# Performance work log

Hardware: AMD Instinct MI355X
Metric: run time of the kernel (lower is better)

Reference implementation:

```python
import jax, jax.numpy as jnp
import numpy as np

N, E, D, C = 40000, 640000, 128, 64


def setup_inputs() -> dict:
    key = jax.random.key(0)
    ks = jax.random.split(key, 12)
    x = jax.random.normal(ks[0], (N, D), dtype=jnp.float32)
    edge_row = jax.random.randint(ks[1], (E,), 0, N, dtype=jnp.int32)
    edge_col = jax.random.randint(ks[2], (E,), 0, N, dtype=jnp.int32)
    edge_val = jax.random.uniform(ks[3], (E,), dtype=jnp.float32)
    s1 = 1.0 / np.sqrt(D)
    W1 = jax.random.uniform(ks[4], (D, D), minval=-s1, maxval=s1, dtype=jnp.float32)
    b1 = jax.random.uniform(ks[5], (D,), minval=-s1, maxval=s1, dtype=jnp.float32)
    W2 = jax.random.uniform(ks[6], (D, D), minval=-s1, maxval=s1, dtype=jnp.float32)
    b2 = jax.random.uniform(ks[7], (D,), minval=-s1, maxval=s1, dtype=jnp.float32)
    Wf = jax.random.uniform(ks[8], (D, C), minval=-s1, maxval=s1, dtype=jnp.float32)
    bf = jax.random.uniform(ks[9], (C,), minval=-s1, maxval=s1, dtype=jnp.float32)
    return {"x": x, "edge_row": edge_row, "edge_col": edge_col, "edge_val": edge_val,
            "W1": W1, "b1": b1, "W2": W2, "b2": b2, "Wf": Wf, "bf": bf}


def _spmm(row, col, val, dense):
    # out[row] += val * dense[col]  == adj @ dense with adj in COO form
    msgs = dense[col] * val[:, None]  # [E, D]
    return jax.ops.segment_sum(msgs, row, num_segments=N)


def reference(x, edge_row, edge_col, edge_val, W1, b1, W2, b2, Wf, bf):
    # gc1: relu(adj @ (x @ W1) + b1)
    h = jax.nn.relu(_spmm(edge_row, edge_col, edge_val, x @ W1) + b1)
    # dropout(p=0.2, training=False) -> identity in eval mode
    # gc2 + residual: relu(adj @ (h @ W2) + b2) + h
    h2 = jax.nn.relu(_spmm(edge_row, edge_col, edge_val, h @ W2) + b2) + h
    # final linear classifier
    return h2 @ Wf + bf
```

## Files before the change

### kernel.cpp

```cpp
#include <hip/hip_runtime.h>

#define N_NODES 40000
#define N_EDGES 640000
#define DIM     128
#define NCLS    64
#define CAP     64
#define CSTRIDE 16

typedef __attribute__((ext_vector_type(8))) short short8v;
typedef __attribute__((ext_vector_type(4))) float f32x4;

__device__ __forceinline__ unsigned short f2bf(float f) {
    unsigned int u = __float_as_uint(f);
    unsigned int r = u + 0x7fffu + ((u >> 16) & 1u);
    return (unsigned short)(r >> 16);
}
__device__ __forceinline__ float bf2f(unsigned int s) {
    return __uint_as_float(s << 16);
}
__device__ __forceinline__ float4 dec4(uint2 u) {
    return make_float4(bf2f(u.x & 0xffffu), bf2f(u.x >> 16),
                       bf2f(u.y & 0xffffu), bf2f(u.y >> 16));
}

__launch_bounds__(256)
__global__ void prep(const float* __restrict__ W1, const float* __restrict__ W2,
                     const float* __restrict__ Wf,
                     unsigned short* __restrict__ wt1, unsigned short* __restrict__ wt2,
                     unsigned short* __restrict__ wtf, int* __restrict__ counts) {
    const int b = blockIdx.x, tid = threadIdx.x;
    if (b < 2500) {
        counts[b * 256 + tid] = 0;
    } else if (b < 2564) {
        int e = (b - 2500) * 256 + tid;
        int k = e >> 7, n = e & 127;
        wt1[n * 128 + k] = f2bf(W1[e]);
    } else if (b < 2628) {
        int e = (b - 2564) * 256 + tid;
        int k = e >> 7, n = e & 127;
        wt2[n * 128 + k] = f2bf(W2[e]);
    } else {
        int e = (b - 2628) * 256 + tid;
        int k = e >> 6, n = e & 63;
        wtf[n * 128 + k] = f2bf(Wf[e]);
    }
}

__launch_bounds__(256)
__global__ void build_bucket(const int4* __restrict__ erow4, const int4* __restrict__ ecol4,
                             const float4* __restrict__ ev4, int* __restrict__ counts,
                             uint2* __restrict__ bslot) {
    int t = blockIdx.x * 256 + threadIdx.x;
    int4   r = erow4[t];
    int4   c = ecol4[t];
    float4 v = ev4[t];
    int p0 = atomicAdd(&counts[r.x * CSTRIDE], 1);
    int p1 = atomicAdd(&counts[r.y * CSTRIDE], 1);
    int p2 = atomicAdd(&counts[r.z * CSTRIDE], 1);
    int p3 = atomicAdd(&counts[r.w * CSTRIDE], 1);
    if (p0 < CAP) bslot[(size_t)r.x * CAP + p0] = make_uint2((unsigned)c.x, __float_as_uint(v.x));
    if (p1 < CAP) bslot[(size_t)r.y * CAP + p1] = make_uint2((unsigned)c.y, __float_as_uint(v.y));
    if (p2 < CAP) bslot[(size_t)r.z * CAP + p2] = make_uint2((unsigned)c.z, __float_as_uint(v.z));
    if (p3 < CAP) bslot[(size_t)r.w * CAP + p3] = make_uint2((unsigned)c.w, __float_as_uint(v.w));
}

__launch_bounds__(256)
__global__ void gemm_f32A_bf16(const float* __restrict__ A,
                               const unsigned short* __restrict__ WT,
                               unsigned short* __restrict__ C) {
    __shared__ unsigned short sB[128 * 128];
    const int tid = threadIdx.x;
    for (int c = tid; c < 2048; c += 256) {
        int n = c >> 4, j = c & 15;
        short8v v = *reinterpret_cast<const short8v*>(WT + n * 128 + 8 * j);
        *reinterpret_cast<short8v*>(&sB[n * 128 + 8 * (j ^ (n & 7))]) = v;
    }
    __syncthreads();

    const int lane = tid & 63;
    const int wv   = tid >> 6;
    const int m0   = blockIdx.x * 64 + wv * 16;
    const int r    = lane & 15;
    const int g    = lane >> 4;

    short8v af[4];
    const float* arow = A + (size_t)(m0 + r) * 128 + 8 * g;
#pragma unroll
    for (int f = 0; f < 4; ++f) {
        float4 p = *reinterpret_cast<const float4*>(arow + 32 * f);
        float4 q = *reinterpret_cast<const float4*>(arow + 32 * f + 4);
        short8v a;
        a[0] = (short)f2bf(p.x); a[1] = (short)f2bf(p.y);
        a[2] = (short)f2bf(p.z); a[3] = (short)f2bf(p.w);
        a[4] = (short)f2bf(q.x); a[5] = (short)f2bf(q.y);
        a[6] = (short)f2bf(q.z); a[7] = (short)f2bf(q.w);
        af[f] = a;
    }

    f32x4 acc[8];
#pragma unroll
    for (int nt = 0; nt < 8; ++nt) acc[nt] = (f32x4){0.f, 0.f, 0.f, 0.f};

#pragma unroll
    for (int nt = 0; nt < 8; ++nt) {
        const int rw = nt * 16 + r;
        const unsigned short* bbase = &sB[rw * 128];
#pragma unroll
        for (int f = 0; f < 4; ++f) {
            short8v bfr = *reinterpret_cast<const short8v*>(bbase + 8 * ((4 * f + g) ^ (rw & 7)));
            acc[nt] = __builtin_amdgcn_mfma_f32_16x16x32_bf16(af[f], bfr, acc[nt], 0, 0, 0);
        }
    }
#pragma unroll
    for (int nt = 0; nt < 8; ++nt)
#pragma unroll
        for (int rr = 0; rr < 4; ++rr)
            C[(size_t)(m0 + g * 4 + rr) * 128 + nt * 16 + r] = f2bf(acc[nt][rr]);
}

__launch_bounds__(256)
__global__ void gemm_bf16_128(const unsigned short* __restrict__ A,
                              const unsigned short* __restrict__ WT,
                              unsigned short* __restrict__ C) {
    __shared__ unsigned short sB[128 * 128];
    const int tid = threadIdx.x;
    for (int c = tid; c < 2048; c += 256) {
        int n = c >> 4, j = c & 15;
        short8v v = *reinterpret_cast<const short8v*>(WT + n * 128 + 8 * j);
        *reinterpret_cast<short8v*>(&sB[n * 128 + 8 * (j ^ (n & 7))]) = v;
    }
    __syncthreads();

    const int lane = tid & 63;
    const int wv   = tid >> 6;
    const int m0   = blockIdx.x * 64 + wv * 16;
    const int r    = lane & 15;
    const int g    = lane >> 4;

    short8v af[4];
    const unsigned short* arow = A + (size_t)(m0 + r) * 128 + 8 * g;
#pragma unroll
    for (int f = 0; f < 4; ++f)
        af[f] = *reinterpret_cast<const short8v*>(arow + 32 * f);

    f32x4 acc[8];
#pragma unroll
    for (int nt = 0; nt < 8; ++nt) acc[nt] = (f32x4){0.f, 0.f, 0.f, 0.f};

#pragma unroll
    for (int nt = 0; nt < 8; ++nt) {
        const int rw = nt * 16 + r;
        const unsigned short* bbase = &sB[rw * 128];
#pragma unroll
        for (int f = 0; f < 4; ++f) {
            short8v bfr = *reinterpret_cast<const short8v*>(bbase + 8 * ((4 * f + g) ^ (rw & 7)));
            acc[nt] = __builtin_amdgcn_mfma_f32_16x16x32_bf16(af[f], bfr, acc[nt], 0, 0, 0);
        }
    }
#pragma unroll
    for (int nt = 0; nt < 8; ++nt)
#pragma unroll
        for (int rr = 0; rr < 4; ++rr)
            C[(size_t)(m0 + g * 4 + rr) * 128 + nt * 16 + r] = f2bf(acc[nt][rr]);
}

__launch_bounds__(256)
__global__ void gemm_bf16_final(const unsigned short* __restrict__ A,
                                const unsigned short* __restrict__ WT,
                                const float* __restrict__ bias,
                                float* __restrict__ C) {
    __shared__ unsigned short sB[64 * 128];
    const int tid = threadIdx.x;
    for (int c = tid; c < 1024; c += 256) {
        int n = c >> 4, j = c & 15;
        short8v v = *reinterpret_cast<const short8v*>(WT + n * 128 + 8 * j);
        *reinterpret_cast<short8v*>(&sB[n * 128 + 8 * (j ^ (n & 7))]) = v;
    }
    __syncthreads();

    const int lane = tid & 63;
    const int wv   = tid >> 6;
    const int m0   = blockIdx.x * 64 + wv * 16;
    const int r    = lane & 15;
    const int g    = lane >> 4;

    short8v af[4];
    const unsigned short* arow = A + (size_t)(m0 + r) * 128 + 8 * g;
#pragma unroll
    for (int f = 0; f < 4; ++f)
        af[f] = *reinterpret_cast<const short8v*>(arow + 32 * f);

    f32x4 acc[4];
#pragma unroll
    for (int nt = 0; nt < 4; ++nt) acc[nt] = (f32x4){0.f, 0.f, 0.f, 0.f};

#pragma unroll
    for (int nt = 0; nt < 4; ++nt) {
        const int rw = nt * 16 + r;
        const unsigned short* bbase = &sB[rw * 128];
#pragma unroll
        for (int f = 0; f < 4; ++f) {
            short8v bfr = *reinterpret_cast<const short8v*>(bbase + 8 * ((4 * f + g) ^ (rw & 7)));
            acc[nt] = __builtin_amdgcn_mfma_f32_16x16x32_bf16(af[f], bfr, acc[nt], 0, 0, 0);
        }
    }
#pragma unroll
    for (int nt = 0; nt < 4; ++nt)
#pragma unroll
        for (int rr = 0; rr < 4; ++rr)
            C[(size_t)(m0 + g * 4 + rr) * 64 + nt * 16 + r] = acc[nt][rr] + bias[nt * 16 + r];
}

__launch_bounds__(256)
__global__ void spmm_fused_bf16(const uint2* __restrict__ dense2,
                                const uint2* __restrict__ bslot,
                                const int* __restrict__ counts,
                                const float4* __restrict__ bias4,
                                const uint2* __restrict__ residbf,
                                uint2* __restrict__ outbf) {
    const int lane = threadIdx.x & 63;
    const int half = lane >> 5;
    const int sub  = lane & 31;
    const int row  = blockIdx.x * 4 + (threadIdx.x >> 6);
    int deg = counts[row * CSTRIDE];
    if (deg > CAP) deg = CAP;

    int   colr = 0;
    float valr = 0.f;
    if (lane < deg) {
        uint2 s = bslot[(size_t)row * CAP + lane];
        colr = (int)s.x;
        valr = __uint_as_float(s.y);
    }
    const int degUp = (deg + 7) & ~7;

    float ax0 = 0.f, ay0 = 0.f, az0 = 0.f, aw0 = 0.f;
    float ax1 = 0.f, ay1 = 0.f, az1 = 0.f, aw1 = 0.f;
    float ax2 = 0.f, ay2 = 0.f, az2 = 0.f, aw2 = 0.f;
    float ax3 = 0.f, ay3 = 0.f, az3 = 0.f, aw3 = 0.f;
    for (int i = 0; i < degUp; i += 8) {
        int   c0 = __shfl(colr, i + 0 + half); float v0 = __shfl(valr, i + 0 + half);
        int   c1 = __shfl(colr, i + 2 + half); float v1 = __shfl(valr, i + 2 + half);
        int   c2 = __shfl(colr, i + 4 + half); float v2 = __shfl(valr, i + 4 + half);
        int   c3 = __shfl(colr, i + 6 + half); float v3 = __shfl(valr, i + 6 + half);
        uint2 u0 = dense2[(size_t)c0 * 32 + sub];
        uint2 u1 = dense2[(size_t)c1 * 32 + sub];
        uint2 u2 = dense2[(size_t)c2 * 32 + sub];
        uint2 u3 = dense2[(size_t)c3 * 32 + sub];
        float4 d0 = dec4(u0); ax0 += v0 * d0.x; ay0 += v0 * d0.y; az0 += v0 * d0.z; aw0 += v0 * d0.w;
        float4 d1 = dec4(u1); ax1 += v1 * d1.x; ay1 += v1 * d1.y; az1 += v1 * d1.z; aw1 += v1 * d1.w;
        float4 d2 = dec4(u2); ax2 += v2 * d2.x; ay2 += v2 * d2.y; az2 += v2 * d2.z; aw2 += v2 * d2.w;
        float4 d3 = dec4(u3); ax3 += v3 * d3.x; ay3 += v3 * d3.y; az3 += v3 * d3.z; aw3 += v3 * d3.w;
    }
    float sx = (ax0 + ax1) + (ax2 + ax3);
    float sy = (ay0 + ay1) + (ay2 + ay3);
    float sz = (az0 + az1) + (az2 + az3);
    float sw = (aw0 + aw1) + (aw2 + aw3);
    sx += __shfl_xor(sx, 32);
    sy += __shfl_xor(sy, 32);
    sz += __shfl_xor(sz, 32);
    sw += __shfl_xor(sw, 32);

    if (half == 0) {
        float4 bb = bias4[sub];
        sx = fmaxf(sx + bb.x, 0.f);
        sy = fmaxf(sy + bb.y, 0.f);
        sz = fmaxf(sz + bb.z, 0.f);
        sw = fmaxf(sw + bb.w, 0.f);
        if (residbf) {
            float4 rr = dec4(residbf[(size_t)row * 32 + sub]);
            sx += rr.x; sy += rr.y; sz += rr.z; sw += rr.w;
        }
        outbf[(size_t)row * 32 + sub] =
            make_uint2((unsigned)f2bf(sx) | ((unsigned)f2bf(sy) << 16),
                       (unsigned)f2bf(sz) | ((unsigned)f2bf(sw) << 16));
    }
}

extern "C" void kernel_launch(void* const* d_in, const int* in_sizes, int n_in,
                              void* d_out, int out_size, void* d_ws, size_t ws_size,
                              hipStream_t stream) {
    const float* x    = (const float*)d_in[0];
    const int*   erow = (const int*)  d_in[1];
    const int*   ecol = (const int*)  d_in[2];
    const float* ev   = (const float*)d_in[3];
    const float* W1   = (const float*)d_in[4];
    const float* b1   = (const float*)d_in[5];
    const float* W2   = (const float*)d_in[6];
    const float* b2   = (const float*)d_in[7];
    const float* Wf   = (const float*)d_in[8];
    const float* bf   = (const float*)d_in[9];
    float* out = (float*)d_out;

    const size_t MB = 1u << 20;
    char* ws = (char*)d_ws;
    int*            counts = (int*)           (ws + 0 * MB);
    uint2*          bslot  = (uint2*)         (ws + 4 * MB);
    unsigned short* gb     = (unsigned short*)(ws + 25 * MB);
    unsigned short* hb     = (unsigned short*)(ws + 36 * MB);
    unsigned short* h2b    = (unsigned short*)(ws + 47 * MB);
    unsigned short* wt1    = (unsigned short*)(ws + 58 * MB);
    unsigned short* wt2    = (unsigned short*)(ws + 58 * MB + 65536);
    unsigned short* wtf    = (unsigned short*)(ws + 58 * MB + 131072);

    prep<<<2660, 256, 0, stream>>>(W1, W2, Wf, wt1, wt2, wtf, counts);
    build_bucket<<<N_EDGES / 4 / 256, 256, 0, stream>>>(
        (const int4*)erow, (const int4*)ecol, (const float4*)ev, counts, bslot);

    gemm_f32A_bf16<<<N_NODES / 64, 256, 0, stream>>>(x, wt1, gb);
    spmm_fused_bf16<<<N_NODES / 4, 256, 0, stream>>>((const uint2*)gb, bslot, counts,
                                                     (const float4*)b1, nullptr,
                                                     (uint2*)hb);
    gemm_bf16_128<<<N_NODES / 64, 256, 0, stream>>>(hb, wt2, gb);
    spmm_fused_bf16<<<N_NODES / 4, 256, 0, stream>>>((const uint2*)gb, bslot, counts,
                                                     (const float4*)b2, (const uint2*)hb,
                                                     (uint2*)h2b);
    gemm_bf16_final<<<N_NODES / 64, 256, 0, stream>>>(h2b, wtf, bf, out);
}
```

Baseline: 189.7 us.

## Bucket each row's edges into four column-range groups for gather locality

```diff
diff --git a/kernel.cpp b/kernel.cpp
--- a/kernel.cpp
+++ b/kernel.cpp
@@ -4,7 +4,8 @@
 #define N_EDGES 640000
 #define DIM     128
 #define NCLS    64
-#define CAP     64
+#define GCAP    32
+#define NSLOT   128
 #define CSTRIDE 16
 
 typedef __attribute__((ext_vector_type(8))) short short8v;
@@ -54,14 +55,18 @@
     int4   r = erow4[t];
     int4   c = ecol4[t];
     float4 v = ev4[t];
-    int p0 = atomicAdd(&counts[r.x * CSTRIDE], 1);
-    int p1 = atomicAdd(&counts[r.y * CSTRIDE], 1);
-    int p2 = atomicAdd(&counts[r.z * CSTRIDE], 1);
-    int p3 = atomicAdd(&counts[r.w * CSTRIDE], 1);
-    if (p0 < CAP) bslot[(size_t)r.x * CAP + p0] = make_uint2((unsigned)c.x, __float_as_uint(v.x));
-    if (p1 < CAP) bslot[(size_t)r.y * CAP + p1] = make_uint2((unsigned)c.y, __float_as_uint(v.y));
-    if (p2 < CAP) bslot[(size_t)r.z * CAP + p2] = make_uint2((unsigned)c.z, __float_as_uint(v.z));
-    if (p3 < CAP) bslot[(size_t)r.w * CAP + p3] = make_uint2((unsigned)c.w, __float_as_uint(v.w));
+    int g0 = (c.x >= 10000) + (c.x >= 20000) + (c.x >= 30000);
+    int g1 = (c.y >= 10000) + (c.y >= 20000) + (c.y >= 30000);
+    int g2 = (c.z >= 10000) + (c.z >= 20000) + (c.z >= 30000);
+    int g3 = (c.w >= 10000) + (c.w >= 20000) + (c.w >= 30000);
+    int p0 = atomicAdd(&counts[r.x * CSTRIDE + g0], 1);
+    int p1 = atomicAdd(&counts[r.y * CSTRIDE + g1], 1);
+    int p2 = atomicAdd(&counts[r.z * CSTRIDE + g2], 1);
+    int p3 = atomicAdd(&counts[r.w * CSTRIDE + g3], 1);
+    if (p0 < GCAP) bslot[(size_t)r.x * NSLOT + g0 * GCAP + p0] = make_uint2((unsigned)c.x, __float_as_uint(v.x));
+    if (p1 < GCAP) bslot[(size_t)r.y * NSLOT + g1 * GCAP + p1] = make_uint2((unsigned)c.y, __float_as_uint(v.y));
+    if (p2 < GCAP) bslot[(size_t)r.z * NSLOT + g2 * GCAP + p2] = make_uint2((unsigned)c.z, __float_as_uint(v.z));
+    if (p3 < GCAP) bslot[(size_t)r.w * NSLOT + g3 * GCAP + p3] = make_uint2((unsigned)c.w, __float_as_uint(v.w));
 }
 
 __launch_bounds__(256)
@@ -222,13 +227,20 @@
     const int half = lane >> 5;
     const int sub  = lane & 31;
     const int row  = blockIdx.x * 4 + (threadIdx.x >> 6);
-    int deg = counts[row * CSTRIDE];
-    if (deg > CAP) deg = CAP;
+
+    int4 cnt = *reinterpret_cast<const int4*>(&counts[row * CSTRIDE]);
+    const int c0 = min(cnt.x, GCAP), c1 = min(cnt.y, GCAP);
+    const int c2 = min(cnt.z, GCAP), c3 = min(cnt.w, GCAP);
+    const int off1 = c0, off2 = c0 + c1, off3 = c0 + c1 + c2;
+    int deg = off3 + c3;
+    if (deg > 64) deg = 64;
 
     int   colr = 0;
     float valr = 0.f;
     if (lane < deg) {
-        uint2 s = bslot[(size_t)row * CAP + lane];
+        int g = (lane >= off1) + (lane >= off2) + (lane >= off3);
+        int base = (g == 0) ? 0 : ((g == 1) ? off1 : ((g == 2) ? off2 : off3));
+        uint2 s = bslot[(size_t)row * NSLOT + g * GCAP + (lane - base)];
         colr = (int)s.x;
         valr = __uint_as_float(s.y);
     }
@@ -239,14 +251,14 @@
     float ax2 = 0.f, ay2 = 0.f, az2 = 0.f, aw2 = 0.f;
     float ax3 = 0.f, ay3 = 0.f, az3 = 0.f, aw3 = 0.f;
     for (int i = 0; i < degUp; i += 8) {
-        int   c0 = __shfl(colr, i + 0 + half); float v0 = __shfl(valr, i + 0 + half);
-        int   c1 = __shfl(colr, i + 2 + half); float v1 = __shfl(valr, i + 2 + half);
-        int   c2 = __shfl(colr, i + 4 + half); float v2 = __shfl(valr, i + 4 + half);
-        int   c3 = __shfl(colr, i + 6 + half); float v3 = __shfl(valr, i + 6 + half);
-        uint2 u0 = dense2[(size_t)c0 * 32 + sub];
-        uint2 u1 = dense2[(size_t)c1 * 32 + sub];
-        uint2 u2 = dense2[(size_t)c2 * 32 + sub];
-        uint2 u3 = dense2[(size_t)c3 * 32 + sub];
+        int   c0e = __shfl(colr, i + 0 + half); float v0 = __shfl(valr, i + 0 + half);
+        int   c1e = __shfl(colr, i + 2 + half); float v1 = __shfl(valr, i + 2 + half);
+        int   c2e = __shfl(colr, i + 4 + half); float v2 = __shfl(valr, i + 4 + half);
+        int   c3e = __shfl(colr, i + 6 + half); float v3 = __shfl(valr, i + 6 + half);
+        uint2 u0 = dense2[(size_t)c0e * 32 + sub];
+        uint2 u1 = dense2[(size_t)c1e * 32 + sub];
+        uint2 u2 = dense2[(size_t)c2e * 32 + sub];
+        uint2 u3 = dense2[(size_t)c3e * 32 + sub];
         float4 d0 = dec4(u0); ax0 += v0 * d0.x; ay0 += v0 * d0.y; az0 += v0 * d0.z; aw0 += v0 * d0.w;
         float4 d1 = dec4(u1); ax1 += v1 * d1.x; ay1 += v1 * d1.y; az1 += v1 * d1.z; aw1 += v1 * d1.w;
         float4 d2 = dec4(u2); ax2 += v2 * d2.x; ay2 += v2 * d2.y; az2 += v2 * d2.z; aw2 += v2 * d2.w;
@@ -296,12 +308,12 @@
     char* ws = (char*)d_ws;
     int*            counts = (int*)           (ws + 0 * MB);
     uint2*          bslot  = (uint2*)         (ws + 4 * MB);
-    unsigned short* gb     = (unsigned short*)(ws + 25 * MB);
-    unsigned short* hb     = (unsigned short*)(ws + 36 * MB);
-    unsigned short* h2b    = (unsigned short*)(ws + 47 * MB);
-    unsigned short* wt1    = (unsigned short*)(ws + 58 * MB);
-    unsigned short* wt2    = (unsigned short*)(ws + 58 * MB + 65536);
-    unsigned short* wtf    = (unsigned short*)(ws + 58 * MB + 131072);
+    unsigned short* gb     = (unsigned short*)(ws + 46 * MB);
+    unsigned short* hb     = (unsigned short*)(ws + 57 * MB);
+    unsigned short* h2b    = (unsigned short*)(ws + 68 * MB);
+    unsigned short* wt1    = (unsigned short*)(ws + 79 * MB);
+    unsigned short* wt2    = (unsigned short*)(ws + 79 * MB + 65536);
+    unsigned short* wtf    = (unsigned short*)(ws + 79 * MB + 131072);
 
     prep<<<2660, 256, 0, stream>>>(W1, W2, Wf, wt1, wt2, wtf, counts);
     build_bucket<<<N_EDGES / 4 / 256, 256, 0, stream>>>(
```

Measured after the change: 191.8 us. Within noise of the previous version (+1.1%).

## Merge edge bucketing, first GEMM and weight prep into one heterogeneous launch

Applied to the files above, without the earlier changes.

```diff
diff --git a/kernel.cpp b/kernel.cpp
--- a/kernel.cpp
+++ b/kernel.cpp
@@ -7,6 +7,11 @@
 #define CAP     64
 #define CSTRIDE 16
 
+#define NB_BUILD 625
+#define NB_GEMM  625
+#define NB_WT2   64
+#define NB_WTF   32
+
 typedef __attribute__((ext_vector_type(8))) short short8v;
 typedef __attribute__((ext_vector_type(4))) float f32x4;
 
@@ -24,98 +29,93 @@
 }
 
 __launch_bounds__(256)
-__global__ void prep(const float* __restrict__ W1, const float* __restrict__ W2,
-                     const float* __restrict__ Wf,
-                     unsigned short* __restrict__ wt1, unsigned short* __restrict__ wt2,
-                     unsigned short* __restrict__ wtf, int* __restrict__ counts) {
-    const int b = blockIdx.x, tid = threadIdx.x;
-    if (b < 2500) {
-        counts[b * 256 + tid] = 0;
-    } else if (b < 2564) {
-        int e = (b - 2500) * 256 + tid;
-        int k = e >> 7, n = e & 127;
-        wt1[n * 128 + k] = f2bf(W1[e]);
-    } else if (b < 2628) {
-        int e = (b - 2564) * 256 + tid;
+__global__ void prep_wt1(const float* __restrict__ W1, unsigned short* __restrict__ wt1) {
+    int e = blockIdx.x * 256 + threadIdx.x;
+    int k = e >> 7, n = e & 127;
+    wt1[n * 128 + k] = f2bf(W1[e]);
+}
+
+__launch_bounds__(256)
+__global__ void build_and_gemm1(const int4* __restrict__ erow4, const int4* __restrict__ ecol4,
+                                const float4* __restrict__ ev4, int* __restrict__ counts,
+                                uint2* __restrict__ bslot,
+                                const float* __restrict__ A,
+                                const unsigned short* __restrict__ WT1,
+                                unsigned short* __restrict__ C,
+                                const float* __restrict__ W2, const float* __restrict__ Wf,
+                                unsigned short* __restrict__ wt2,
+                                unsigned short* __restrict__ wtf) {
+    const int bid = blockIdx.x, tid = threadIdx.x;
+    if (bid < NB_BUILD) {
+        int t = bid * 256 + tid;
+        int4   r = erow4[t];
+        int4   c = ecol4[t];
+        float4 v = ev4[t];
+        int p0 = atomicAdd(&counts[r.x * CSTRIDE], 1);
+        int p1 = atomicAdd(&counts[r.y * CSTRIDE], 1);
+        int p2 = atomicAdd(&counts[r.z * CSTRIDE], 1);
+        int p3 = atomicAdd(&counts[r.w * CSTRIDE], 1);
+        if (p0 < CAP) bslot[(size_t)r.x * CAP + p0] = make_uint2((unsigned)c.x, __float_as_uint(v.x));
+        if (p1 < CAP) bslot[(size_t)r.y * CAP + p1] = make_uint2((unsigned)c.y, __float_as_uint(v.y));
+        if (p2 < CAP) bslot[(size_t)r.z * CAP + p2] = make_uint2((unsigned)c.z, __float_as_uint(v.z));
+        if (p3 < CAP) bslot[(size_t)r.w * CAP + p3] = make_uint2((unsigned)c.w, __float_as_uint(v.w));
+    } else if (bid < NB_BUILD + NB_GEMM) {
+        __shared__ unsigned short sB[128 * 128];
+        for (int c = tid; c < 2048; c += 256) {
+            int n = c >> 4, j = c & 15;
+            short8v v = *reinterpret_cast<const short8v*>(WT1 + n * 128 + 8 * j);
+            *reinterpret_cast<short8v*>(&sB[n * 128 + 8 * (j ^ (n & 7))]) = v;
+        }
+        __syncthreads();
+
+        const int lane = tid & 63;
+        const int wv   = tid >> 6;
+        const int m0   = (bid - NB_BUILD) * 64 + wv * 16;
+        const int r    = lane & 15;
+        const int g    = lane >> 4;
+
+        short8v af[4];
+        const float* arow = A + (size_t)(m0 + r) * 128 + 8 * g;
+#pragma unroll
+        for (int f = 0; f < 4; ++f) {
+            float4 p = *reinterpret_cast<const float4*>(arow + 32 * f);
+            float4 q = *reinterpret_cast<const float4*>(arow + 32 * f + 4);
+            short8v a;
+            a[0] = (short)f2bf(p.x); a[1] = (short)f2bf(p.y);
+            a[2] = (short)f2bf(p.z); a[3] = (short)f2bf(p.w);
+            a[4] = (short)f2bf(q.x); a[5] = (short)f2bf(q.y);
+            a[6] = (short)f2bf(q.z); a[7] = (short)f2bf(q.w);
+            af[f] = a;
+        }
+
+        f32x4 acc[8];
+#pragma unroll
+        for (int nt = 0; nt < 8; ++nt) acc[nt] = (f32x4){0.f, 0.f, 0.f, 0.f};
+
+#pragma unroll
+        for (int nt = 0; nt < 8; ++nt) {
+            const int rw = nt * 16 + r;
+            const unsigned short* bbase = &sB[rw * 128];
+#pragma unroll
+            for (int f = 0; f < 4; ++f) {
+                short8v bfr = *reinterpret_cast<const short8v*>(bbase + 8 * ((4 * f + g) ^ (rw & 7)));
+                acc[nt] = __builtin_amdgcn_mfma_f32_16x16x32_bf16(af[f], bfr, acc[nt], 0, 0, 0);
+            }
+        }
+#pragma unroll
+        for (int nt = 0; nt < 8; ++nt)
+#pragma unroll
+            for (int rr = 0; rr < 4; ++rr)
+                C[(size_t)(m0 + g * 4 + rr) * 128 + nt * 16 + r] = f2bf(acc[nt][rr]);
+    } else if (bid < NB_BUILD + NB_GEMM + NB_WT2) {
+        int e = (bid - NB_BUILD - NB_GEMM) * 256 + tid;
         int k = e >> 7, n = e & 127;
         wt2[n * 128 + k] = f2bf(W2[e]);
     } else {
-        int e = (b - 2628) * 256 + tid;
+        int e = (bid - NB_BUILD - NB_GEMM - NB_WT2) * 256 + tid;
         int k = e >> 6, n = e & 63;
         wtf[n * 128 + k] = f2bf(Wf[e]);
     }
-}
-
-__launch_bounds__(256)
-__global__ void build_bucket(const int4* __restrict__ erow4, const int4* __restrict__ ecol4,
-                             const float4* __restrict__ ev4, int* __restrict__ counts,
-                             uint2* __restrict__ bslot) {
-    int t = blockIdx.x * 256 + threadIdx.x;
-    int4   r = erow4[t];
-    int4   c = ecol4[t];
-    float4 v = ev4[t];
-    int p0 = atomicAdd(&counts[r.x * CSTRIDE], 1);
-    int p1 = atomicAdd(&counts[r.y * CSTRIDE], 1);
-    int p2 = atomicAdd(&counts[r.z * CSTRIDE], 1);
-    int p3 = atomicAdd(&counts[r.w * CSTRIDE], 1);
-    if (p0 < CAP) bslot[(size_t)r.x * CAP + p0] = make_uint2((unsigned)c.x, __float_as_uint(v.x));
-    if (p1 < CAP) bslot[(size_t)r.y * CAP + p1] = make_uint2((unsigned)c.y, __float_as_uint(v.y));
-    if (p2 < CAP) bslot[(size_t)r.z * CAP + p2] = make_uint2((unsigned)c.z, __float_as_uint(v.z));
-    if (p3 < CAP) bslot[(size_t)r.w * CAP + p3] = make_uint2((unsigned)c.w, __float_as_uint(v.w));
-}
-
-__launch_bounds__(256)
-__global__ void gemm_f32A_bf16(const float* __restrict__ A,
-                               const unsigned short* __restrict__ WT,
-                               unsigned short* __restrict__ C) {
-    __shared__ unsigned short sB[128 * 128];
-    const int tid = threadIdx.x;
-    for (int c = tid; c < 2048; c += 256) {
-        int n = c >> 4, j = c & 15;
-        short8v v = *reinterpret_cast<const short8v*>(WT + n * 128 + 8 * j);
-        *reinterpret_cast<short8v*>(&sB[n * 128 + 8 * (j ^ (n & 7))]) = v;
-    }
-    __syncthreads();
-
-    const int lane = tid & 63;
-    const int wv   = tid >> 6;
-    const int m0   = blockIdx.x * 64 + wv * 16;
-    const int r    = lane & 15;
-    const int g    = lane >> 4;
-
-    short8v af[4];
-    const float* arow = A + (size_t)(m0 + r) * 128 + 8 * g;
-#pragma unroll
-    for (int f = 0; f < 4; ++f) {
-        float4 p = *reinterpret_cast<const float4*>(arow + 32 * f);
-        float4 q = *reinterpret_cast<const float4*>(arow + 32 * f + 4);
-        short8v a;
-        a[0] = (short)f2bf(p.x); a[1] = (short)f2bf(p.y);
-        a[2] = (short)f2bf(p.z); a[3] = (short)f2bf(p.w);
-        a[4] = (short)f2bf(q.x); a[5] = (short)f2bf(q.y);
-        a[6] = (short)f2bf(q.z); a[7] = (short)f2bf(q.w);
-        af[f] = a;
-    }
-
-    f32x4 acc[8];
-#pragma unroll
-    for (int nt = 0; nt < 8; ++nt) acc[nt] = (f32x4){0.f, 0.f, 0.f, 0.f};
-
-#pragma unroll
-    for (int nt = 0; nt < 8; ++nt) {
-        const int rw = nt * 16 + r;
-        const unsigned short* bbase = &sB[rw * 128];
-#pragma unroll
-        for (int f = 0; f < 4; ++f) {
-            short8v bfr = *reinterpret_cast<const short8v*>(bbase + 8 * ((4 * f + g) ^ (rw & 7)));
-            acc[nt] = __builtin_amdgcn_mfma_f32_16x16x32_bf16(af[f], bfr, acc[nt], 0, 0, 0);
-        }
-    }
-#pragma unroll
-    for (int nt = 0; nt < 8; ++nt)
-#pragma unroll
-        for (int rr = 0; rr < 4; ++rr)
-            C[(size_t)(m0 + g * 4 + rr) * 128 + nt * 16 + r] = f2bf(acc[nt][rr]);
 }
 
 __launch_bounds__(256)
@@ -303,11 +303,13 @@
     unsigned short* wt2    = (unsigned short*)(ws + 58 * MB + 65536);
     unsigned short* wtf    = (unsigned short*)(ws + 58 * MB + 131072);
 
-    prep<<<2660, 256, 0, stream>>>(W1, W2, Wf, wt1, wt2, wtf, counts);
-    build_bucket<<<N_EDGES / 4 / 256, 256, 0, stream>>>(
-        (const int4*)erow, (const int4*)ecol, (const float4*)ev, counts, bslot);
-
-    gemm_f32A_bf16<<<N_NODES / 64, 256, 0, stream>>>(x, wt1, gb);
+    hipMemsetAsync(counts, 0, (size_t)N_NODES * CSTRIDE * sizeof(int), stream);
+    prep_wt1<<<64, 256, 0, stream>>>(W1, wt1);
+
+    build_and_gemm1<<<NB_BUILD + NB_GEMM + NB_WT2 + NB_WTF, 256, 0, stream>>>(
+        (const int4*)erow, (const int4*)ecol, (const float4*)ev, counts, bslot,
+        x, wt1, gb, W2, Wf, wt2, wtf);
+
     spmm_fused_bf16<<<N_NODES / 4, 256, 0, stream>>>((const uint2*)gb, bslot, counts,
                                                      (const float4*)b1, nullptr,
                                                      (uint2*)hb);
```

Result: slower. 194.6 us (+2.6%).
